# Optimization experiments

Hardware: AMD Instinct MI355X
Metric: run time of the kernel (lower is better)

The kernel has to match this reference:

```python
import jax, jax.numpy as jnp
import numpy as np

N = 128
NPTS = 120000
G = 64  # voxel grid side


def _build_coords_and_nbrs():
    rng = np.random.default_rng(0)
    lin = rng.choice(G ** 3, size=NPTS, replace=False)
    xs = lin // (G * G)
    ys = (lin // G) % G
    zs = lin % G
    lut = np.full(G ** 3, -1, np.int32)
    lut[lin] = np.arange(NPTS, dtype=np.int32)
    nbr = np.full((NPTS, 27), -1, np.int32)
    k = 0
    for dx in (-1, 0, 1):
        for dy in (-1, 0, 1):
            for dz in (-1, 0, 1):
                nx, ny, nz = xs + dx, ys + dy, zs + dz
                ok = (nx >= 0) & (nx < G) & (ny >= 0) & (ny < G) & (nz >= 0) & (nz < G)
                nl = np.clip(nx * G * G + ny * G + nz, 0, G ** 3 - 1)
                nbr[:, k] = np.where(ok, lut[nl], -1)
                k += 1
    return nbr


def setup_inputs() -> dict:
    key = jax.random.key(0)
    k = jax.random.split(key, 6)
    H = N // 2
    x = jax.random.normal(k[0], (NPTS, N), jnp.float32)
    W1s = jax.random.normal(k[1], (6, N, H), jnp.float32) * np.sqrt(2.0 / N)
    Wks = jax.random.normal(k[2], (6, 27, H, H), jnp.float32) * np.sqrt(2.0 / (27 * H))
    W2s = jax.random.normal(k[3], (6, H, N), jnp.float32) * np.sqrt(1.0 / H)
    Wf = jax.random.normal(k[4], (N, N), jnp.float32) * np.sqrt(1.0 / N)
    nbr_idx = jnp.asarray(_build_coords_and_nbrs())
    return {"x": x, "W1s": W1s, "Wks": Wks, "W2s": W2s, "Wf": Wf, "nbr_idx": nbr_idx}


def reference(x, W1s, Wks, W2s, Wf, nbr_idx):
    valid = nbr_idx >= 0                      # [NPTS, 27]
    safe = jnp.maximum(nbr_idx, 0)

    def conv3(h, Wk):
        # gather-matmul-scatter over the 27 coordinate offsets (as ME does)
        out = jnp.zeros((h.shape[0], Wk.shape[2]), h.dtype)
        for kk in range(27):
            g = jnp.where(valid[:, kk, None], h[safe[:, kk]], 0.0)
            out = out + g @ Wk[kk]
        return out

    def residual_unit(h, i):
        t = jax.nn.relu(h @ W1s[i])           # 1x1 conv N -> N/2
        t = jax.nn.relu(conv3(t, Wks[i]))     # 3^3 sparse conv N/2 -> N/2
        t = t @ W2s[i]                        # 1x1 conv N/2 -> N
        return jax.nn.relu(t + h)

    a = x
    for i in range(3):
        a = residual_unit(a, i)
    b = x
    for i in range(3, 6):
        b = residual_unit(b, i)
    b = b @ Wf                                # final 1x1 conv in branch b
    return a * jax.nn.sigmoid(b) + x
```

## Files before the change

### kernel.cpp

```cpp
#include <hip/hip_runtime.h>
#include <stdint.h>

#define NPTS 120000

typedef __attribute__((ext_vector_type(8))) short bf16x8;
typedef __attribute__((ext_vector_type(4))) float f32x4;

__device__ __forceinline__ uint16_t f2b(float f) {
    union { float f; uint32_t i; } v; v.f = f;
    uint32_t x = v.i;
    return (uint16_t)((x + 0x7fffu + ((x >> 16) & 1u)) >> 16);
}
__device__ __forceinline__ float b2f(uint16_t u) {
    union { uint32_t i; float f; } v; v.i = ((uint32_t)u) << 16; return v.f;
}
__device__ __forceinline__ bf16x8 cvt8(f32x4 a, f32x4 b) {
    bf16x8 t;
    t[0] = (short)f2b(a[0]); t[1] = (short)f2b(a[1]);
    t[2] = (short)f2b(a[2]); t[3] = (short)f2b(a[3]);
    t[4] = (short)f2b(b[0]); t[5] = (short)f2b(b[1]);
    t[6] = (short)f2b(b[2]); t[7] = (short)f2b(b[3]);
    return t;
}
#define MFMA(a, b, c) __builtin_amdgcn_mfma_f32_16x16x32_bf16((a), (b), (c), 0, 0, 0)

__global__ __launch_bounds__(256) void k_swz(
    const float* __restrict__ W1s, const float* __restrict__ Wks,
    const float* __restrict__ W2s, const float* __restrict__ Wf,
    uint16_t* __restrict__ Z, uint16_t* __restrict__ T1z)
{
    if (blockIdx.x == 0 && threadIdx.x < 64)
        T1z[(size_t)NPTS * 64 + threadIdx.x] = 0;
    int idx = blockIdx.x * 256 + threadIdx.x;
    if (idx >= 778240) return;
    const float* src; int K, N, r;
    if (idx < 49152)       { src = W1s + (idx / 8192) * 8192;           K = 128; N = 64;  r = idx & 8191; }
    else if (idx < 712704) { int t = idx - 49152;  src = Wks + (t >> 12) * 4096; K = 64;  N = 64;  r = t & 4095; }
    else if (idx < 761856) { int t = idx - 712704; src = W2s + (t / 8192) * 8192; K = 64;  N = 128; r = t & 8191; }
    else                   { src = Wf; K = 128; N = 128; r = idx - 761856; }
    int j  = r & 7;
    int l  = (r >> 3) & 63;
    int t2 = r >> 9;
    int KC = K >> 5;
    int kc = t2 % KC;
    int nt = t2 / KC;
    int k  = kc * 32 + (l >> 4) * 8 + j;
    int n  = nt * 16 + (l & 15);
    Z[idx] = f2b(src[k * N + n]);
}

__global__ __launch_bounds__(256) void k_nbrT(
    const int* __restrict__ nbr, int* __restrict__ nbrT)
{
    __shared__ int st[27 * 64];
    const int tid = threadIdx.x;
    const long p0 = (long)blockIdx.x * 64;
    for (int i = tid; i < 1728; i += 256) {
        int lp = i / 27, kk = i - lp * 27;
        int n = nbr[p0 * 27 + i];
        st[kk * 64 + lp] = ((n < 0) ? NPTS : n) << 6;
    }
    __syncthreads();
    for (int i = tid; i < 1728; i += 256) {
        int kk = i >> 6, lp = i & 63;
        nbrT[(long)kk * NPTS + p0 + lp] = st[i];
    }
}

__global__ __launch_bounds__(256) void k_gemm1(
    const float* __restrict__ H, const uint16_t* __restrict__ Wz,
    uint16_t* __restrict__ T)
{
    const int tid = threadIdx.x;
    const int wv = tid >> 6, ln = tid & 63;
    const int m = ln & 15, part = ln >> 4;
    const long rb = (long)blockIdx.x * 64 + wv * 16;

    bf16x8 a[4];
    const float* hrow = H + (rb + m) * 128 + part * 8;
    #pragma unroll
    for (int kc = 0; kc < 4; ++kc) {
        f32x4 h0 = *reinterpret_cast<const f32x4*>(hrow + kc * 32);
        f32x4 h1 = *reinterpret_cast<const f32x4*>(hrow + kc * 32 + 4);
        a[kc] = cvt8(h0, h1);
    }
    #pragma unroll
    for (int nt = 0; nt < 4; ++nt) {
        f32x4 acc = (f32x4)(0.0f);
        #pragma unroll
        for (int kc = 0; kc < 4; ++kc) {
            bf16x8 b = *reinterpret_cast<const bf16x8*>(Wz + ((nt * 4 + kc) * 64 + ln) * 8);
            acc = MFMA(a[kc], b, acc);
        }
        #pragma unroll
        for (int r = 0; r < 4; ++r) {
            float v = acc[r] > 0.f ? acc[r] : 0.f;
            T[(rb + part * 4 + r) * 64 + nt * 16 + m] = f2b(v);
        }
    }
}

template<int MODE>
__global__ __launch_bounds__(256, (MODE == 2) ? 2 : 3) void k_conv(
    const uint16_t* __restrict__ T,
    const uint16_t* __restrict__ Wkz,
    const uint16_t* __restrict__ W2z,
    const float* Hin,
    const int* __restrict__ nbrT,
    float* HoutF,
    uint16_t* __restrict__ HoutB,
    const uint16_t* __restrict__ Wfz,
    const uint16_t* __restrict__ A16g,
    const float* __restrict__ Xg,
    float* __restrict__ OutF)
{
    constexpr int SLICE_SH = (MODE == 2) ? 6528 : 3456;
    __shared__ __align__(16) uint16_t wkbuf[2][4096];
    __shared__ __align__(16) uint16_t uni[4][SLICE_SH];
    const int tid = threadIdx.x;
    const int wv = tid >> 6, ln = tid & 63;
    const int mrow = ln & 15, part = ln >> 4, pc8 = part * 8;
    const long bb = (long)blockIdx.x * 192;
    const long wb0 = bb + wv * 48;

    {
        const uint16_t* g = Wkz + wv * 1024 + ln * 8;
        bf16x8 s0 = *reinterpret_cast<const bf16x8*>(g);
        bf16x8 s1 = *reinterpret_cast<const bf16x8*>(g + 512);
        *reinterpret_cast<bf16x8*>(&wkbuf[0][wv * 1024 + ln * 8]) = s0;
        *reinterpret_cast<bf16x8*>(&wkbuf[0][wv * 1024 + 512 + ln * 8]) = s1;
    }
    int idx[3];
    #pragma unroll
    for (int mm = 0; mm < 3; ++mm) idx[mm] = nbrT[wb0 + mm * 16 + mrow];
    __syncthreads();

    f32x4 acc[3][4];
    #pragma unroll
    for (int mm = 0; mm < 3; ++mm)
        #pragma unroll
        for (int nt = 0; nt < 4; ++nt) acc[mm][nt] = (f32x4)(0.0f);

    int cur = 0;
    #pragma unroll 1
    for (int k = 0; k < 27; ++k) {
        bf16x8 A[3][2];
        #pragma unroll
        for (int mm = 0; mm < 3; ++mm) {
            const uint16_t* s = T + (long)idx[mm] + pc8;
            A[mm][0] = *reinterpret_cast<const bf16x8*>(s);
            A[mm][1] = *reinterpret_cast<const bf16x8*>(s + 32);
        }
        bf16x8 s0, s1;
        if (k < 26) {
            const uint16_t* g = Wkz + (k + 1) * 4096 + wv * 1024 + ln * 8;
            s0 = *reinterpret_cast<const bf16x8*>(g);
            s1 = *reinterpret_cast<const bf16x8*>(g + 512);
            const int* ib = nbrT + (long)(k + 1) * NPTS + wb0;
            #pragma unroll
            for (int mm = 0; mm < 3; ++mm) idx[mm] = ib[mm * 16 + mrow];
        }
        bf16x8 B[8];
        #pragma unroll
        for (int i = 0; i < 8; ++i)
            B[i] = *reinterpret_cast<const bf16x8*>(&wkbuf[cur][i * 512 + ln * 8]);
        #pragma unroll
        for (int nt = 0; nt < 4; ++nt)
            #pragma unroll
            for (int mm = 0; mm < 3; ++mm) {
                acc[mm][nt] = MFMA(A[mm][0], B[nt * 2 + 0], acc[mm][nt]);
                acc[mm][nt] = MFMA(A[mm][1], B[nt * 2 + 1], acc[mm][nt]);
            }
        if (k < 26) {
            *reinterpret_cast<bf16x8*>(&wkbuf[cur ^ 1][wv * 1024 + ln * 8]) = s0;
            *reinterpret_cast<bf16x8*>(&wkbuf[cur ^ 1][wv * 1024 + 512 + ln * 8]) = s1;
        }
        __syncthreads();
        cur ^= 1;
    }

    uint16_t* sc2 = &uni[wv][0];
    #pragma unroll
    for (int mm = 0; mm < 3; ++mm)
        #pragma unroll
        for (int nt = 0; nt < 4; ++nt)
            #pragma unroll
            for (int r = 0; r < 4; ++r) {
                float v = acc[mm][nt][r];
                v = v > 0.f ? v : 0.f;
                sc2[(mm * 16 + part * 4 + r) * 72 + nt * 16 + mrow] = f2b(v);
            }
    __builtin_amdgcn_wave_barrier();

    bf16x8 a2[3][2];
    #pragma unroll
    for (int mm = 0; mm < 3; ++mm) {
        const uint16_t* crow = sc2 + (mm * 16 + mrow) * 72;
        a2[mm][0] = *reinterpret_cast<const bf16x8*>(crow + pc8);
        a2[mm][1] = *reinterpret_cast<const bf16x8*>(crow + 32 + pc8);
    }
    __builtin_amdgcn_wave_barrier();

    #pragma unroll 2
    for (int nt = 0; nt < 8; ++nt) {
        bf16x8 b0 = *reinterpret_cast<const bf16x8*>(W2z + ((nt * 2 + 0) * 64 + ln) * 8);
        bf16x8 b1 = *reinterpret_cast<const bf16x8*>(W2z + ((nt * 2 + 1) * 64 + ln) * 8);
        f32x4 c[3];
        #pragma unroll
        for (int mm = 0; mm < 3; ++mm) {
            c[mm] = (f32x4)(0.0f);
            c[mm] = MFMA(a2[mm][0], b0, c[mm]);
            c[mm] = MFMA(a2[mm][1], b1, c[mm]);
        }
        const int col = nt * 16 + mrow;
        if (MODE == 0) {
            #pragma unroll
            for (int mm = 0; mm < 3; ++mm)
                #pragma unroll
                for (int r = 0; r < 4; ++r) {
                    long p = wb0 + mm * 16 + part * 4 + r;
                    float v = c[mm][r] + Hin[p * 128 + col];
                    HoutF[p * 128 + col] = v > 0.f ? v : 0.f;
                }
        } else if (MODE == 1) {
            #pragma unroll
            for (int mm = 0; mm < 3; ++mm)
                #pragma unroll
                for (int r = 0; r < 4; ++r) {
                    long p = wb0 + mm * 16 + part * 4 + r;
                    float v = c[mm][r] + Hin[p * 128 + col];
                    v = v > 0.f ? v : 0.f;
                    HoutB[p * 128 + col] = f2b(v);
                }
        } else {
            uint16_t* sH = &uni[wv][0];
            #pragma unroll
            for (int mm = 0; mm < 3; ++mm)
                #pragma unroll
                for (int r = 0; r < 4; ++r) {
                    long p = wb0 + mm * 16 + part * 4 + r;
                    float v = c[mm][r] + Hin[p * 128 + col];
                    v = v > 0.f ? v : 0.f;
                    sH[(mm * 16 + part * 4 + r) * 136 + col] = f2b(v);
                }
        }
    }

    if (MODE == 2) {
        __builtin_amdgcn_wave_barrier();
        const uint16_t* sH = &uni[wv][0];
        bf16x8 af[3][4];
        #pragma unroll
        for (int mm = 0; mm < 3; ++mm)
            #pragma unroll
            for (int kc = 0; kc < 4; ++kc)
                af[mm][kc] = *reinterpret_cast<const bf16x8*>(
                    sH + (mm * 16 + mrow) * 136 + kc * 32 + pc8);
        #pragma unroll 2
        for (int nt = 0; nt < 8; ++nt) {
            f32x4 fa[3] = { (f32x4)(0.f), (f32x4)(0.f), (f32x4)(0.f) };
            #pragma unroll
            for (int kc = 0; kc < 4; ++kc) {
                bf16x8 b = *reinterpret_cast<const bf16x8*>(Wfz + ((nt * 4 + kc) * 64 + ln) * 8);
                #pragma unroll
                for (int mm = 0; mm < 3; ++mm)
                    fa[mm] = MFMA(af[mm][kc], b, fa[mm]);
            }
            const int col = nt * 16 + mrow;
            #pragma unroll
            for (int mm = 0; mm < 3; ++mm)
                #pragma unroll
                for (int r = 0; r < 4; ++r) {
                    long p = wb0 + mm * 16 + part * 4 + r;
                    float s = 1.f / (1.f + __expf(-fa[mm][r]));
                    OutF[p * 128 + col] = b2f(A16g[p * 128 + col]) * s + Xg[p * 128 + col];
                }
        }
    }
}

extern "C" void kernel_launch(void* const* d_in, const int* in_sizes, int n_in,
                              void* d_out, int out_size, void* d_ws, size_t ws_size,
                              hipStream_t stream)
{
    const float* x   = (const float*)d_in[0];
    const float* W1s = (const float*)d_in[1];
    const float* Wks = (const float*)d_in[2];
    const float* W2s = (const float*)d_in[3];
    const float* Wf  = (const float*)d_in[4];
    const int*   nbr = (const int*)d_in[5];
    float*       out = (float*)d_out;

    uint16_t* A16 = (uint16_t*)d_ws;
    uint16_t* T1  = A16 + (size_t)NPTS * 128;
    uint16_t* Z   = T1 + (size_t)(NPTS + 1) * 64;
    int* nbrT     = (int*)(Z + 778240);
    const uint16_t* W1z = Z;
    const uint16_t* Wkz = Z + 49152;
    const uint16_t* W2z = Z + 712704;
    const uint16_t* Wfz = Z + 761856;

    k_swz <<<dim3(3040), dim3(256), 0, stream>>>(W1s, Wks, W2s, Wf, Z, T1);
    k_nbrT<<<dim3(1875), dim3(256), 0, stream>>>(nbr, nbrT);

    auto g1 = [&](int i, const float* h) {
        k_gemm1<<<dim3(1875), dim3(256), 0, stream>>>(h, W1z + (size_t)i * 8192, T1);
    };

    g1(0, x);
    k_conv<0><<<dim3(625), dim3(256), 0, stream>>>(T1, Wkz + 0 * 110592, W2z + 0 * 8192,
        x,   nbrT, out, nullptr, nullptr, nullptr, nullptr, nullptr);
    g1(1, out);
    k_conv<0><<<dim3(625), dim3(256), 0, stream>>>(T1, Wkz + 1 * 110592, W2z + 1 * 8192,
        out, nbrT, out, nullptr, nullptr, nullptr, nullptr, nullptr);
    g1(2, out);
    k_conv<1><<<dim3(625), dim3(256), 0, stream>>>(T1, Wkz + 2 * 110592, W2z + 2 * 8192,
        out, nbrT, nullptr, A16, nullptr, nullptr, nullptr, nullptr);
    g1(3, x);
    k_conv<0><<<dim3(625), dim3(256), 0, stream>>>(T1, Wkz + 3 * 110592, W2z + 3 * 8192,
        x,   nbrT, out, nullptr, nullptr, nullptr, nullptr, nullptr);
    g1(4, out);
    k_conv<0><<<dim3(625), dim3(256), 0, stream>>>(T1, Wkz + 4 * 110592, W2z + 4 * 8192,
        out, nbrT, out, nullptr, nullptr, nullptr, nullptr, nullptr);
    g1(5, out);
    k_conv<2><<<dim3(625), dim3(256), 0, stream>>>(T1, Wkz + 5 * 110592, W2z + 5 * 8192,
        out, nbrT, nullptr, nullptr, Wfz, A16, x, out);
}
```

Measured before the change: 675.5 us.

## Run both residual branches concurrently in paired kernels and software-pipeline gathers

The two independent residual branches (a and b) now run side by side: each launch of the gemm1 and conv kernels covers both branches, which doubles the grid and halves the number of serial launches. Branch a gets its own fp32 buffer and T buffer in the workspace. The conv tap loop is unrolled by two with explicit ping-pong registers so the gather for the next tap is issued before the MFMAs of the current one. The final Wf gemm and sigmoid gating move from the MODE 2 conv epilogue into a separate k_final kernel, and a fallback path keeps the sequential schedule when the workspace is too small. The costs are extra workspace and an extra read/write pass for the final gating step.

```diff
diff --git a/kernel.cpp b/kernel.cpp
--- a/kernel.cpp
+++ b/kernel.cpp
@@ -27,10 +27,15 @@
 __global__ __launch_bounds__(256) void k_swz(
     const float* __restrict__ W1s, const float* __restrict__ Wks,
     const float* __restrict__ W2s, const float* __restrict__ Wf,
-    uint16_t* __restrict__ Z, uint16_t* __restrict__ T1z)
-{
-    if (blockIdx.x == 0 && threadIdx.x < 64)
-        T1z[(size_t)NPTS * 64 + threadIdx.x] = 0;
+    uint16_t* __restrict__ Z, uint16_t* __restrict__ T1z,
+    uint16_t* __restrict__ T2z)
+{
+    if (blockIdx.x == 0) {
+        if (threadIdx.x < 64)
+            T1z[(size_t)NPTS * 64 + threadIdx.x] = 0;
+        else if (threadIdx.x < 128 && T2z)
+            T2z[(size_t)NPTS * 64 + (threadIdx.x - 64)] = 0;
+    }
     int idx = blockIdx.x * 256 + threadIdx.x;
     if (idx >= 778240) return;
     const float* src; int K, N, r;
@@ -67,14 +72,14 @@
     }
 }
 
-__global__ __launch_bounds__(256) void k_gemm1(
-    const float* __restrict__ H, const uint16_t* __restrict__ Wz,
+__device__ __forceinline__ void gemm1_body(
+    int b, const float* __restrict__ H, const uint16_t* __restrict__ Wz,
     uint16_t* __restrict__ T)
 {
     const int tid = threadIdx.x;
     const int wv = tid >> 6, ln = tid & 63;
     const int m = ln & 15, part = ln >> 4;
-    const long rb = (long)blockIdx.x * 64 + wv * 16;
+    const long rb = (long)b * 64 + wv * 16;
 
     bf16x8 a[4];
     const float* hrow = H + (rb + m) * 128 + part * 8;
@@ -89,8 +94,8 @@
         f32x4 acc = (f32x4)(0.0f);
         #pragma unroll
         for (int kc = 0; kc < 4; ++kc) {
-            bf16x8 b = *reinterpret_cast<const bf16x8*>(Wz + ((nt * 4 + kc) * 64 + ln) * 8);
-            acc = MFMA(a[kc], b, acc);
+            bf16x8 b8 = *reinterpret_cast<const bf16x8*>(Wz + ((nt * 4 + kc) * 64 + ln) * 8);
+            acc = MFMA(a[kc], b8, acc);
         }
         #pragma unroll
         for (int r = 0; r < 4; ++r) {
@@ -100,86 +105,121 @@
     }
 }
 
+__global__ __launch_bounds__(256) void k_gemm1(
+    const float* __restrict__ H, const uint16_t* __restrict__ Wz,
+    uint16_t* __restrict__ T)
+{
+    gemm1_body(blockIdx.x, H, Wz, T);
+}
+
+__global__ __launch_bounds__(256) void k_gemm1p(
+    const float* __restrict__ HA, const float* __restrict__ HB,
+    const uint16_t* __restrict__ WzA, const uint16_t* __restrict__ WzB,
+    uint16_t* __restrict__ TA, uint16_t* __restrict__ TB)
+{
+    int b = blockIdx.x;
+    if (b < 1875) gemm1_body(b, HA, WzA, TA);
+    else          gemm1_body(b - 1875, HB, WzB, TB);
+}
+
+struct SM {
+    uint16_t wkbuf[2][4096];
+    uint16_t uni[4][3456];
+};
+
+__device__ __forceinline__ void gather6(bf16x8 (&dst)[3][2], const int (&ix)[3],
+                                        const uint16_t* __restrict__ T, int pc8)
+{
+    #pragma unroll
+    for (int mm = 0; mm < 3; ++mm) {
+        const uint16_t* s = T + (long)ix[mm] + pc8;
+        dst[mm][0] = *reinterpret_cast<const bf16x8*>(s);
+        dst[mm][1] = *reinterpret_cast<const bf16x8*>(s + 32);
+    }
+}
+__device__ __forceinline__ void ldidx(int (&ix)[3], const int* __restrict__ p, int mrow)
+{
+    #pragma unroll
+    for (int mm = 0; mm < 3; ++mm) ix[mm] = p[mm * 16 + mrow];
+}
+__device__ __forceinline__ void pload(bf16x8& s0, bf16x8& s1, const uint16_t* __restrict__ g)
+{
+    s0 = *reinterpret_cast<const bf16x8*>(g);
+    s1 = *reinterpret_cast<const bf16x8*>(g + 512);
+}
+__device__ __forceinline__ void tap24(f32x4 (&acc)[3][4], const bf16x8 (&A)[3][2],
+                                      const uint16_t* wk, int ln)
+{
+    bf16x8 B[8];
+    #pragma unroll
+    for (int i = 0; i < 8; ++i)
+        B[i] = *reinterpret_cast<const bf16x8*>(wk + i * 512 + ln * 8);
+    #pragma unroll
+    for (int nt = 0; nt < 4; ++nt)
+        #pragma unroll
+        for (int mm = 0; mm < 3; ++mm) {
+            acc[mm][nt] = MFMA(A[mm][0], B[nt * 2 + 0], acc[mm][nt]);
+            acc[mm][nt] = MFMA(A[mm][1], B[nt * 2 + 1], acc[mm][nt]);
+        }
+}
+
 template<int MODE>
-__global__ __launch_bounds__(256, (MODE == 2) ? 2 : 3) void k_conv(
-    const uint16_t* __restrict__ T,
-    const uint16_t* __restrict__ Wkz,
-    const uint16_t* __restrict__ W2z,
-    const float* Hin,
-    const int* __restrict__ nbrT,
-    float* HoutF,
-    uint16_t* __restrict__ HoutB,
-    const uint16_t* __restrict__ Wfz,
-    const uint16_t* __restrict__ A16g,
-    const float* __restrict__ Xg,
-    float* __restrict__ OutF)
-{
-    constexpr int SLICE_SH = (MODE == 2) ? 6528 : 3456;
-    __shared__ __align__(16) uint16_t wkbuf[2][4096];
-    __shared__ __align__(16) uint16_t uni[4][SLICE_SH];
+__device__ __forceinline__ void conv_body(
+    SM& sm, int blk,
+    const uint16_t* __restrict__ T, const uint16_t* __restrict__ Wkz,
+    const uint16_t* __restrict__ W2z, const float* Hin,
+    const int* __restrict__ nbrT, float* HoutF, uint16_t* __restrict__ HoutB)
+{
     const int tid = threadIdx.x;
     const int wv = tid >> 6, ln = tid & 63;
     const int mrow = ln & 15, part = ln >> 4, pc8 = part * 8;
-    const long bb = (long)blockIdx.x * 192;
+    const long bb = (long)blk * 192;
     const long wb0 = bb + wv * 48;
 
     {
-        const uint16_t* g = Wkz + wv * 1024 + ln * 8;
-        bf16x8 s0 = *reinterpret_cast<const bf16x8*>(g);
-        bf16x8 s1 = *reinterpret_cast<const bf16x8*>(g + 512);
-        *reinterpret_cast<bf16x8*>(&wkbuf[0][wv * 1024 + ln * 8]) = s0;
-        *reinterpret_cast<bf16x8*>(&wkbuf[0][wv * 1024 + 512 + ln * 8]) = s1;
-    }
-    int idx[3];
-    #pragma unroll
-    for (int mm = 0; mm < 3; ++mm) idx[mm] = nbrT[wb0 + mm * 16 + mrow];
+        bf16x8 s0, s1;
+        pload(s0, s1, Wkz + wv * 1024 + ln * 8);
+        *reinterpret_cast<bf16x8*>(&sm.wkbuf[0][wv * 1024 + ln * 8]) = s0;
+        *reinterpret_cast<bf16x8*>(&sm.wkbuf[0][wv * 1024 + 512 + ln * 8]) = s1;
+    }
+    int ixA[3], ixB[3];
+    bf16x8 pA[3][2], pB[3][2];
+    ldidx(ixA, nbrT + wb0, mrow);
+    gather6(pA, ixA, T, pc8);
+    ldidx(ixB, nbrT + (long)NPTS + wb0, mrow);
+
+    f32x4 acc[3][4];
+    #pragma unroll
+    for (int mm = 0; mm < 3; ++mm)
+        #pragma unroll
+        for (int nt = 0; nt < 4; ++nt) acc[mm][nt] = (f32x4)(0.0f);
     __syncthreads();
 
-    f32x4 acc[3][4];
-    #pragma unroll
-    for (int mm = 0; mm < 3; ++mm)
-        #pragma unroll
-        for (int nt = 0; nt < 4; ++nt) acc[mm][nt] = (f32x4)(0.0f);
-
-    int cur = 0;
     #pragma unroll 1
-    for (int k = 0; k < 27; ++k) {
-        bf16x8 A[3][2];
-        #pragma unroll
-        for (int mm = 0; mm < 3; ++mm) {
-            const uint16_t* s = T + (long)idx[mm] + pc8;
-            A[mm][0] = *reinterpret_cast<const bf16x8*>(s);
-            A[mm][1] = *reinterpret_cast<const bf16x8*>(s + 32);
-        }
+    for (int t = 0; t < 26; t += 2) {
         bf16x8 s0, s1;
-        if (k < 26) {
-            const uint16_t* g = Wkz + (k + 1) * 4096 + wv * 1024 + ln * 8;
-            s0 = *reinterpret_cast<const bf16x8*>(g);
-            s1 = *reinterpret_cast<const bf16x8*>(g + 512);
-            const int* ib = nbrT + (long)(k + 1) * NPTS + wb0;
-            #pragma unroll
-            for (int mm = 0; mm < 3; ++mm) idx[mm] = ib[mm * 16 + mrow];
-        }
-        bf16x8 B[8];
-        #pragma unroll
-        for (int i = 0; i < 8; ++i)
-            B[i] = *reinterpret_cast<const bf16x8*>(&wkbuf[cur][i * 512 + ln * 8]);
-        #pragma unroll
-        for (int nt = 0; nt < 4; ++nt)
-            #pragma unroll
-            for (int mm = 0; mm < 3; ++mm) {
-                acc[mm][nt] = MFMA(A[mm][0], B[nt * 2 + 0], acc[mm][nt]);
-                acc[mm][nt] = MFMA(A[mm][1], B[nt * 2 + 1], acc[mm][nt]);
-            }
-        if (k < 26) {
-            *reinterpret_cast<bf16x8*>(&wkbuf[cur ^ 1][wv * 1024 + ln * 8]) = s0;
-            *reinterpret_cast<bf16x8*>(&wkbuf[cur ^ 1][wv * 1024 + 512 + ln * 8]) = s1;
-        }
+        gather6(pB, ixB, T, pc8);
+        pload(s0, s1, Wkz + (t + 1) * 4096 + wv * 1024 + ln * 8);
+        if (t + 2 < 27) ldidx(ixA, nbrT + (long)(t + 2) * NPTS + wb0, mrow);
+        tap24(acc, pA, &sm.wkbuf[0][0], ln);
+        *reinterpret_cast<bf16x8*>(&sm.wkbuf[1][wv * 1024 + ln * 8]) = s0;
+        *reinterpret_cast<bf16x8*>(&sm.wkbuf[1][wv * 1024 + 512 + ln * 8]) = s1;
         __syncthreads();
-        cur ^= 1;
-    }
-
-    uint16_t* sc2 = &uni[wv][0];
+        if (t + 1 < 26) {
+            gather6(pA, ixA, T, pc8);
+            pload(s0, s1, Wkz + (t + 2) * 4096 + wv * 1024 + ln * 8);
+            if (t + 3 < 27) ldidx(ixB, nbrT + (long)(t + 3) * NPTS + wb0, mrow);
+        }
+        tap24(acc, pB, &sm.wkbuf[1][0], ln);
+        if (t + 1 < 26) {
+            *reinterpret_cast<bf16x8*>(&sm.wkbuf[0][wv * 1024 + ln * 8]) = s0;
+            *reinterpret_cast<bf16x8*>(&sm.wkbuf[0][wv * 1024 + 512 + ln * 8]) = s1;
+        }
+        __syncthreads();
+    }
+    tap24(acc, pA, &sm.wkbuf[0][0], ln);
+
+    uint16_t* sc2 = &sm.uni[wv][0];
     #pragma unroll
     for (int mm = 0; mm < 3; ++mm)
         #pragma unroll
@@ -222,7 +262,7 @@
                     float v = c[mm][r] + Hin[p * 128 + col];
                     HoutF[p * 128 + col] = v > 0.f ? v : 0.f;
                 }
-        } else if (MODE == 1) {
+        } else {
             #pragma unroll
             for (int mm = 0; mm < 3; ++mm)
                 #pragma unroll
@@ -232,49 +272,69 @@
                     v = v > 0.f ? v : 0.f;
                     HoutB[p * 128 + col] = f2b(v);
                 }
-        } else {
-            uint16_t* sH = &uni[wv][0];
-            #pragma unroll
-            for (int mm = 0; mm < 3; ++mm)
-                #pragma unroll
-                for (int r = 0; r < 4; ++r) {
-                    long p = wb0 + mm * 16 + part * 4 + r;
-                    float v = c[mm][r] + Hin[p * 128 + col];
-                    v = v > 0.f ? v : 0.f;
-                    sH[(mm * 16 + part * 4 + r) * 136 + col] = f2b(v);
-                }
-        }
-    }
-
-    if (MODE == 2) {
-        __builtin_amdgcn_wave_barrier();
-        const uint16_t* sH = &uni[wv][0];
-        bf16x8 af[3][4];
-        #pragma unroll
-        for (int mm = 0; mm < 3; ++mm)
-            #pragma unroll
-            for (int kc = 0; kc < 4; ++kc)
-                af[mm][kc] = *reinterpret_cast<const bf16x8*>(
-                    sH + (mm * 16 + mrow) * 136 + kc * 32 + pc8);
-        #pragma unroll 2
-        for (int nt = 0; nt < 8; ++nt) {
-            f32x4 fa[3] = { (f32x4)(0.f), (f32x4)(0.f), (f32x4)(0.f) };
-            #pragma unroll
-            for (int kc = 0; kc < 4; ++kc) {
-                bf16x8 b = *reinterpret_cast<const bf16x8*>(Wfz + ((nt * 4 + kc) * 64 + ln) * 8);
-                #pragma unroll
-                for (int mm = 0; mm < 3; ++mm)
-                    fa[mm] = MFMA(af[mm][kc], b, fa[mm]);
-            }
-            const int col = nt * 16 + mrow;
-            #pragma unroll
-            for (int mm = 0; mm < 3; ++mm)
-                #pragma unroll
-                for (int r = 0; r < 4; ++r) {
-                    long p = wb0 + mm * 16 + part * 4 + r;
-                    float s = 1.f / (1.f + __expf(-fa[mm][r]));
-                    OutF[p * 128 + col] = b2f(A16g[p * 128 + col]) * s + Xg[p * 128 + col];
-                }
+        }
+    }
+}
+
+template<int MODE>
+__global__ __launch_bounds__(256, 3) void k_conv1(
+    const uint16_t* __restrict__ T, const uint16_t* __restrict__ Wkz,
+    const uint16_t* __restrict__ W2z, const float* Hin,
+    const int* __restrict__ nbrT, float* HoutF, uint16_t* __restrict__ HoutB)
+{
+    __shared__ SM sm;
+    conv_body<MODE>(sm, blockIdx.x, T, Wkz, W2z, Hin, nbrT, HoutF, HoutB);
+}
+
+template<int MA, int MB>
+__global__ __launch_bounds__(256, 3) void k_convp(
+    const uint16_t* __restrict__ Ta, const uint16_t* __restrict__ Tb,
+    const uint16_t* __restrict__ WkzA, const uint16_t* __restrict__ WkzB,
+    const uint16_t* __restrict__ W2zA, const uint16_t* __restrict__ W2zB,
+    const float* HinA, const float* HinB,
+    const int* __restrict__ nbrT,
+    float* HoFA, float* HoFB,
+    uint16_t* __restrict__ HoBA, uint16_t* __restrict__ HoBB)
+{
+    __shared__ SM sm;
+    int b = blockIdx.x;
+    if (b < 625) conv_body<MA>(sm, b, Ta, WkzA, W2zA, HinA, nbrT, HoFA, HoBA);
+    else         conv_body<MB>(sm, b - 625, Tb, WkzB, W2zB, HinB, nbrT, HoFB, HoBB);
+}
+
+__global__ __launch_bounds__(256) void k_final(
+    const float* B, const uint16_t* __restrict__ Wfz,
+    const uint16_t* __restrict__ A16, const float* __restrict__ X,
+    float* Out)
+{
+    const int tid = threadIdx.x;
+    const int wv = tid >> 6, ln = tid & 63;
+    const int m = ln & 15, part = ln >> 4;
+    const long rb = (long)blockIdx.x * 64 + wv * 16;
+
+    bf16x8 a[4];
+    const float* brow = B + (rb + m) * 128 + part * 8;
+    #pragma unroll
+    for (int kc = 0; kc < 4; ++kc) {
+        f32x4 h0 = *reinterpret_cast<const f32x4*>(brow + kc * 32);
+        f32x4 h1 = *reinterpret_cast<const f32x4*>(brow + kc * 32 + 4);
+        a[kc] = cvt8(h0, h1);
+    }
+    #pragma unroll
+    for (int nt = 0; nt < 8; ++nt) {
+        f32x4 acc = (f32x4)(0.0f);
+        #pragma unroll
+        for (int kc = 0; kc < 4; ++kc) {
+            bf16x8 b = *reinterpret_cast<const bf16x8*>(Wfz + ((nt * 4 + kc) * 64 + ln) * 8);
+            acc = MFMA(a[kc], b, acc);
+        }
+        #pragma unroll
+        for (int r = 0; r < 4; ++r) {
+            long p = rb + part * 4 + r;
+            int col = nt * 16 + m;
+            float s = 1.f / (1.f + __expf(-acc[r]));
+            float av = b2f(A16[p * 128 + col]);
+            Out[p * 128 + col] = av * s + X[p * 128 + col];
         }
     }
 }
@@ -291,38 +351,67 @@
     const int*   nbr = (const int*)d_in[5];
     float*       out = (float*)d_out;
 
+    const size_t A16_sh = (size_t)NPTS * 128;
+    const size_t T_sh   = (size_t)(NPTS + 1) * 64;
+    const size_t Z_sh   = 778240;
+    const size_t nbrT_i = (size_t)27 * NPTS;
+
     uint16_t* A16 = (uint16_t*)d_ws;
-    uint16_t* T1  = A16 + (size_t)NPTS * 128;
-    uint16_t* Z   = T1 + (size_t)(NPTS + 1) * 64;
-    int* nbrT     = (int*)(Z + 778240);
-    const uint16_t* W1z = Z;
-    const uint16_t* Wkz = Z + 49152;
-    const uint16_t* W2z = Z + 712704;
-    const uint16_t* Wfz = Z + 761856;
-
-    k_swz <<<dim3(3040), dim3(256), 0, stream>>>(W1s, Wks, W2s, Wf, Z, T1);
-    k_nbrT<<<dim3(1875), dim3(256), 0, stream>>>(nbr, nbrT);
-
-    auto g1 = [&](int i, const float* h) {
-        k_gemm1<<<dim3(1875), dim3(256), 0, stream>>>(h, W1z + (size_t)i * 8192, T1);
-    };
-
-    g1(0, x);
-    k_conv<0><<<dim3(625), dim3(256), 0, stream>>>(T1, Wkz + 0 * 110592, W2z + 0 * 8192,
-        x,   nbrT, out, nullptr, nullptr, nullptr, nullptr, nullptr);
-    g1(1, out);
-    k_conv<0><<<dim3(625), dim3(256), 0, stream>>>(T1, Wkz + 1 * 110592, W2z + 1 * 8192,
-        out, nbrT, out, nullptr, nullptr, nullptr, nullptr, nullptr);
-    g1(2, out);
-    k_conv<1><<<dim3(625), dim3(256), 0, stream>>>(T1, Wkz + 2 * 110592, W2z + 2 * 8192,
-        out, nbrT, nullptr, A16, nullptr, nullptr, nullptr, nullptr);
-    g1(3, x);
-    k_conv<0><<<dim3(625), dim3(256), 0, stream>>>(T1, Wkz + 3 * 110592, W2z + 3 * 8192,
-        x,   nbrT, out, nullptr, nullptr, nullptr, nullptr, nullptr);
-    g1(4, out);
-    k_conv<0><<<dim3(625), dim3(256), 0, stream>>>(T1, Wkz + 4 * 110592, W2z + 4 * 8192,
-        out, nbrT, out, nullptr, nullptr, nullptr, nullptr, nullptr);
-    g1(5, out);
-    k_conv<2><<<dim3(625), dim3(256), 0, stream>>>(T1, Wkz + 5 * 110592, W2z + 5 * 8192,
-        out, nbrT, nullptr, nullptr, Wfz, A16, x, out);
-}
+    uint16_t* Ta  = A16 + A16_sh;
+    uint16_t* Tb  = Ta + T_sh;
+    uint16_t* Z   = Tb + T_sh;
+    int* nbrT     = (int*)(Z + Z_sh);
+    float* Ha     = (float*)(nbrT + nbrT_i);
+    size_t need_paired = (size_t)((char*)(Ha + A16_sh) - (char*)d_ws);
+
+    if (ws_size >= need_paired) {
+        const uint16_t* W1z = Z;
+        const uint16_t* Wkz = Z + 49152;
+        const uint16_t* W2z = Z + 712704;
+        const uint16_t* Wfz = Z + 761856;
+
+        k_swz <<<dim3(3040), dim3(256), 0, stream>>>(W1s, Wks, W2s, Wf, Z, Ta, Tb);
+        k_nbrT<<<dim3(1875), dim3(256), 0, stream>>>(nbr, nbrT);
+
+        k_gemm1p<<<dim3(3750), dim3(256), 0, stream>>>(x, x, W1z, W1z + 3 * 8192, Ta, Tb);
+        k_convp<0, 0><<<dim3(1250), dim3(256), 0, stream>>>(
+            Ta, Tb, Wkz + 0 * 110592, Wkz + 3 * 110592, W2z + 0 * 8192, W2z + 3 * 8192,
+            x, x, nbrT, Ha, out, nullptr, nullptr);
+        k_gemm1p<<<dim3(3750), dim3(256), 0, stream>>>(Ha, out, W1z + 1 * 8192, W1z + 4 * 8192, Ta, Tb);
+        k_convp<0, 0><<<dim3(1250), dim3(256), 0, stream>>>(
+            Ta, Tb, Wkz + 1 * 110592, Wkz + 4 * 110592, W2z + 1 * 8192, W2z + 4 * 8192,
+            Ha, out, nbrT, Ha, out, nullptr, nullptr);
+        k_gemm1p<<<dim3(3750), dim3(256), 0, stream>>>(Ha, out, W1z + 2 * 8192, W1z + 5 * 8192, Ta, Tb);
+        k_convp<1, 0><<<dim3(1250), dim3(256), 0, stream>>>(
+            Ta, Tb, Wkz + 2 * 110592, Wkz + 5 * 110592, W2z + 2 * 8192, W2z + 5 * 8192,
+            Ha, out, nbrT, nullptr, out, A16, nullptr);
+        k_final<<<dim3(1875), dim3(256), 0, stream>>>(out, Wfz, A16, x, out);
+    } else {
+        uint16_t* Zs   = Ta + T_sh;
+        int* nbrTs     = (int*)(Zs + Z_sh);
+        const uint16_t* W1z = Zs;
+        const uint16_t* Wkz = Zs + 49152;
+        const uint16_t* W2z = Zs + 712704;
+        const uint16_t* Wfz = Zs + 761856;
+
+        k_swz <<<dim3(3040), dim3(256), 0, stream>>>(W1s, Wks, W2s, Wf, Zs, Ta, nullptr);
+        k_nbrT<<<dim3(1875), dim3(256), 0, stream>>>(nbr, nbrTs);
+
+        auto g1 = [&](int i, const float* h) {
+            k_gemm1<<<dim3(1875), dim3(256), 0, stream>>>(h, W1z + (size_t)i * 8192, Ta);
+        };
+        g1(0, x);
+        k_conv1<0><<<dim3(625), dim3(256), 0, stream>>>(Ta, Wkz + 0 * 110592, W2z + 0 * 8192, x,   nbrTs, out, nullptr);
+        g1(1, out);
+        k_conv1<0><<<dim3(625), dim3(256), 0, stream>>>(Ta, Wkz + 1 * 110592, W2z + 1 * 8192, out, nbrTs, out, nullptr);
+        g1(2, out);
+        k_conv1<1><<<dim3(625), dim3(256), 0, stream>>>(Ta, Wkz + 2 * 110592, W2z + 2 * 8192, out, nbrTs, nullptr, A16);
+        g1(3, x);
+        k_conv1<0><<<dim3(625), dim3(256), 0, stream>>>(Ta, Wkz + 3 * 110592, W2z + 3 * 8192, x,   nbrTs, out, nullptr);
+        g1(4, out);
+        k_conv1<0><<<dim3(625), dim3(256), 0, stream>>>(Ta, Wkz + 4 * 110592, W2z + 4 * 8192, out, nbrTs, out, nullptr);
+        g1(5, out);
+        k_conv1<0><<<dim3(625), dim3(256), 0, stream>>>(Ta, Wkz + 5 * 110592, W2z + 5 * 8192, out, nbrTs, out, nullptr);
+        k_final<<<dim3(1875), dim3(256), 0, stream>>>(out, Wfz, A16, x, out);
+    }
+}
```

After: 666.8 us. No clear change (-1.3%).
